# Optimization experiments

Hardware: AMD Instinct MI355X
Metric: run time of the kernel (lower is better)

## Reference

```python
import jax, jax.numpy as jnp
import numpy as np

N = 50000   # nodes
E = 800000  # edges
H = 4       # num_heads
D = 32      # out_dim
IN = 256    # in_dim


def setup_inputs() -> dict:
    key = jax.random.key(0)
    k0, k1, k2, k3, k4, k5 = jax.random.split(key, 6)
    h = jax.random.normal(k0, (N, IN), dtype=jnp.float32)
    # fl weight (torch Linear stores [out, in]), xavier-ish scale
    Wl = jax.random.normal(k1, (H * D, IN), dtype=jnp.float32) * (1.0 / np.sqrt(IN))
    # fc / fq are initialized to small constants in torch; use small random here
    fc = jax.random.normal(k2, (IN, H * D), dtype=jnp.float32) * 0.02
    fq = jax.random.normal(k3, (IN, H * D), dtype=jnp.float32) * 0.02
    src = jax.random.randint(k4, (E,), 0, N)
    dst = jax.random.randint(k5, (E,), 0, N)
    return {"h": h, "Wl": Wl, "fc": fc, "fq": fq, "src": src, "dst": dst}


def reference(h, Wl, fc, fq, src, dst):
    n = h.shape[0]
    ft = (h @ Wl.T).reshape(n, H, D)      # [N,H,D]
    ft_c = (h @ fc).reshape(n, H, D)      # [N,H,D]
    ft_q = (h @ fq).reshape(n, H, D)      # [N,H,D]

    # edge attention: c = ft_c[dst], q = ft_q[src] - c, a = ELU(sum(q*c))
    c = ft_c[dst]                         # [E,H,D]
    a = jax.nn.elu(jnp.sum((ft_q[src] - c) * c, axis=-1))  # [E,H]

    # segmented (per-destination) softmax over incoming edges, per head
    m = jax.ops.segment_max(a, dst, num_segments=n)        # [N,H]
    ex = jnp.exp(a - m[dst])
    s = jax.ops.segment_sum(ex, dst, num_segments=n)       # [N,H]
    attn = ex / s[dst]                                     # [E,H]

    # global top-k (smallest l_s) threshold + mass redistribution, per head
    l_s = int(0.713 * attn.shape[0])
    srt = jnp.sort(attn, axis=0)                           # ascending per head
    thd = srt[l_s - 1]                                     # [H] l_s-th smallest
    topk_sum = jnp.sum(srt[:l_s], axis=0)                  # [H]
    a2 = jnp.where(attn - thd < 0, jnp.zeros((), attn.dtype), attn)
    ratio = (jnp.sum(a2, axis=0) + topk_sum) / jnp.sum(a2, axis=0)  # [H]
    a3 = a2 * ratio                                        # [E,H]

    # weighted scatter-sum of source features to destinations
    out = jax.ops.segment_sum(ft[src] * a3[:, :, None], dst, num_segments=n)  # [N,H,D]

    # concat=True: cat(flattened heads, mean over heads of ft)
    return jnp.concatenate([out.reshape(n, -1), ft.mean(axis=1)], axis=1)  # [N, H*D + D]
```

## Files before the change

### kernel.cpp

```cpp
#include <hip/hip_runtime.h>
#include <hip/hip_bf16.h>
#include <math.h>

#define N_NODES 50000
#define N_EDGES 800000
#define NH 4
#define DH 32
#define IN_DIM 256
#define OUTC 160
#define LS 570400
#define RANK0 (LS - 1)

typedef unsigned long long u64;
#define SC_FX 1099511627776.0

__device__ __forceinline__ unsigned enc_f(float a){
  unsigned u = __float_as_uint(a);
  return (u & 0x80000000u) ? ~u : (u | 0x80000000u);
}
__device__ __forceinline__ float dec_f(unsigned k){
  return (k & 0x80000000u) ? __uint_as_float(k ^ 0x80000000u) : __uint_as_float(~k);
}

__global__ void k_prepw1(const float* __restrict__ Wl, float* __restrict__ W1){
  int i = blockIdx.x * 256 + threadIdx.x;
  if (i >= IN_DIM * 128) return;
  int k = i >> 7, j = i & 127;
  W1[i] = Wl[j * IN_DIM + k];
}
__global__ void k_prepw2(const float* __restrict__ fc, const float* __restrict__ fq,
                         double* __restrict__ W2){
  int i = blockIdx.x * 256 + threadIdx.x;
  if (i >= IN_DIM * 256) return;
  int k = i >> 8, j = i & 255;
  W2[i] = (double)((j < 128) ? fc[k * 128 + j] : fq[k * 128 + (j - 128)]);
}

#define BM 128
#define BK 16
__global__ __launch_bounds__(256) void k_gemm32(const float* __restrict__ A,
                                                const float* __restrict__ W1,
                                                float* __restrict__ C){
  __shared__ float As[BK][BM + 4];
  __shared__ float Bs[BK][128 + 4];
  int tid = threadIdx.x;
  int m0 = blockIdx.x * BM;
  int ty = tid / 16, tx = tid % 16;
  float acc[8][8];
  #pragma unroll
  for (int i = 0; i < 8; i++)
    #pragma unroll
    for (int j = 0; j < 8; j++) acc[i][j] = 0.f;

  for (int k0 = 0; k0 < IN_DIM; k0 += BK){
    #pragma unroll
    for (int i = 0; i < 2; i++){
      int s = tid * 2 + i;
      int row = s >> 2, c4 = s & 3;
      int r = m0 + row;
      float4 v = make_float4(0.f, 0.f, 0.f, 0.f);
      if (r < N_NODES) v = *(const float4*)&A[(size_t)r * IN_DIM + k0 + c4 * 4];
      As[c4 * 4 + 0][row] = v.x; As[c4 * 4 + 1][row] = v.y;
      As[c4 * 4 + 2][row] = v.z; As[c4 * 4 + 3][row] = v.w;
    }
    #pragma unroll
    for (int i = 0; i < 2; i++){
      int s = tid * 2 + i;
      int kr = s >> 5, c4 = s & 31;
      if (c4 < 32){
        float4 v = *(const float4*)&W1[(size_t)(k0 + kr) * 128 + c4 * 4];
        *(float4*)&Bs[kr][c4 * 4] = v;
      }
    }
    __syncthreads();
    #pragma unroll
    for (int kk = 0; kk < BK; kk++){
      float4 a0 = *(const float4*)&As[kk][ty * 4];
      float4 a1 = *(const float4*)&As[kk][64 + ty * 4];
      float4 b0 = *(const float4*)&Bs[kk][tx * 4];
      float4 b1 = *(const float4*)&Bs[kk][64 + tx * 4];
      float av[8] = {a0.x, a0.y, a0.z, a0.w, a1.x, a1.y, a1.z, a1.w};
      float bv[8] = {b0.x, b0.y, b0.z, b0.w, b1.x, b1.y, b1.z, b1.w};
      #pragma unroll
      for (int i = 0; i < 8; i++)
        #pragma unroll
        for (int j = 0; j < 8; j++)
          acc[i][j] = fmaf(av[i], bv[j], acc[i][j]);
    }
    __syncthreads();
  }
  #pragma unroll
  for (int i = 0; i < 8; i++){
    int r = m0 + ((i < 4) ? (ty * 4 + i) : (64 + ty * 4 + (i - 4)));
    if (r >= N_NODES) continue;
    *(float4*)&C[(size_t)r * 128 + tx * 4]      = make_float4(acc[i][0], acc[i][1], acc[i][2], acc[i][3]);
    *(float4*)&C[(size_t)r * 128 + 64 + tx * 4] = make_float4(acc[i][4], acc[i][5], acc[i][6], acc[i][7]);
  }
}

__global__ __launch_bounds__(256) void k_gemm64(const float* __restrict__ A,
                                                const double* __restrict__ W2,
                                                double* __restrict__ C){
  __shared__ double As[16][66];
  __shared__ double Bs[16][66];
  int tid = threadIdx.x;
  int m0 = blockIdx.x * 64;
  int n0 = blockIdx.y * 64;
  int ty = tid / 16, tx = tid % 16;
  double acc[4][4];
  #pragma unroll
  for (int i = 0; i < 4; i++)
    #pragma unroll
    for (int j = 0; j < 4; j++) acc[i][j] = 0.0;

  for (int k0 = 0; k0 < IN_DIM; k0 += 16){
    {
      int row = tid >> 2, c4 = tid & 3;
      int r = m0 + row;
      float4 v = make_float4(0.f, 0.f, 0.f, 0.f);
      if (r < N_NODES) v = *(const float4*)&A[(size_t)r * IN_DIM + k0 + c4 * 4];
      As[c4 * 4 + 0][row] = (double)v.x; As[c4 * 4 + 1][row] = (double)v.y;
      As[c4 * 4 + 2][row] = (double)v.z; As[c4 * 4 + 3][row] = (double)v.w;
    }
    {
      int kr = tid >> 4, c4 = tid & 15;
      const double* p = &W2[(size_t)(k0 + kr) * 256 + n0 + c4 * 4];
      double2 b0 = *(const double2*)p;
      double2 b1 = *(const double2*)(p + 2);
      Bs[kr][c4 * 4 + 0] = b0.x; Bs[kr][c4 * 4 + 1] = b0.y;
      Bs[kr][c4 * 4 + 2] = b1.x; Bs[kr][c4 * 4 + 3] = b1.y;
    }
    __syncthreads();
    #pragma unroll
    for (int kk = 0; kk < 16; kk++){
      double a[4], b[4];
      #pragma unroll
      for (int i = 0; i < 4; i++) a[i] = As[kk][ty * 4 + i];
      #pragma unroll
      for (int j = 0; j < 4; j++) b[j] = Bs[kk][tx * 4 + j];
      #pragma unroll
      for (int i = 0; i < 4; i++)
        #pragma unroll
        for (int j = 0; j < 4; j++)
          acc[i][j] = fma(a[i], b[j], acc[i][j]);
    }
    __syncthreads();
  }
  #pragma unroll
  for (int i = 0; i < 4; i++){
    int r = m0 + ty * 4 + i;
    if (r >= N_NODES) continue;
    double* p = &C[(size_t)r * 256 + n0 + tx * 4];
    *(double2*)p       = make_double2(acc[i][0], acc[i][1]);
    *(double2*)(p + 2) = make_double2(acc[i][2], acc[i][3]);
  }
}

__global__ void k_mean(const float* __restrict__ ft, float* __restrict__ out){
  int i = blockIdx.x * 256 + threadIdx.x;
  if (i >= N_NODES * DH) return;
  int n = i / DH, dd = i % DH;
  const float* p = ft + (size_t)n * 128;
  out[(size_t)n * OUTC + 128 + dd] = 0.25f * (p[dd] + p[32 + dd] + p[64 + dd] + p[96 + dd]);
}

__global__ __launch_bounds__(256) void k_edge_a(const double* __restrict__ fcq,
    const int* __restrict__ src, const int* __restrict__ dst,
    double* __restrict__ abuf, unsigned* __restrict__ menc){
  int wid = blockIdx.x * 4 + (threadIdx.x >> 6);
  int t = threadIdx.x & 63;
  if (wid >= N_EDGES) return;
  int s = src[wid], d = dst[wid];
  const double* qp = fcq + (size_t)s * 256 + 128;
  const double* cp = fcq + (size_t)d * 256;
  double2 q = *(const double2*)&qp[t * 2];
  double2 c = *(const double2*)&cp[t * 2];
  double val = (q.x - c.x) * c.x + (q.y - c.y) * c.y;
  val += __shfl_xor(val, 1);
  val += __shfl_xor(val, 2);
  val += __shfl_xor(val, 4);
  val += __shfl_xor(val, 8);
  if ((t & 15) == 0){
    int hh = t >> 4;
    double a = (val > 0.0) ? val : expm1(val);
    abuf[(size_t)wid * 4 + hh] = a;
    atomicMax(&menc[(size_t)d * 4 + hh], enc_f((float)a));
  }
}

__global__ void k_ex_sum(const int* __restrict__ dst, double* __restrict__ abuf,
                         const unsigned* __restrict__ menc, u64* __restrict__ ssum64){
  int i = blockIdx.x * 256 + threadIdx.x;
  if (i >= N_EDGES * 4) return;
  int e = i >> 2, hh = i & 3;
  int d = dst[e];
  double m = (double)dec_f(menc[(size_t)d * 4 + hh]);
  double ex = exp(abuf[i] - m);
  abuf[i] = ex;
  atomicAdd(&ssum64[(size_t)d * 4 + hh], (u64)llrint(ex * SC_FX));
}

__global__ void k_attn(const int* __restrict__ dst, double* __restrict__ abuf,
                       const u64* __restrict__ ssum64){
  int i = blockIdx.x * 256 + threadIdx.x;
  if (i >= N_EDGES * 4) return;
  int e = i >> 2, hh = i & 3;
  double s = (double)ssum64[(size_t)dst[e] * 4 + hh] * (1.0 / SC_FX);
  abuf[i] = abuf[i] / s;
}

__global__ void k_deg(const int* __restrict__ dst, unsigned* __restrict__ deg){
  int e = blockIdx.x * 256 + threadIdx.x;
  if (e < N_EDGES) atomicAdd(&deg[dst[e]], 1u);
}

__global__ __launch_bounds__(1024) void k_scan(const unsigned* __restrict__ deg,
                                               unsigned* __restrict__ offsets){
  __shared__ unsigned ps[1024];
  int t = threadIdx.x;
  const int CH = (N_NODES + 1023) / 1024;
  int base = t * CH;
  unsigned s = 0;
  for (int i = 0; i < CH; i++){
    int n = base + i;
    if (n < N_NODES) s += deg[n];
  }
  ps[t] = s;
  __syncthreads();
  for (int off = 1; off < 1024; off <<= 1){
    unsigned v = (t >= off) ? ps[t - off] : 0;
    __syncthreads();
    ps[t] += v;
    __syncthreads();
  }
  unsigned ex = (t == 0) ? 0 : ps[t - 1];
  for (int i = 0; i < CH; i++){
    int n = base + i;
    if (n < N_NODES){ offsets[n] = ex; ex += deg[n]; }
  }
  if (t == 1023) offsets[N_NODES] = ps[1023];
}

__global__ void k_cpcur(const unsigned* __restrict__ offsets, unsigned* __restrict__ cur){
  int i = blockIdx.x * 256 + threadIdx.x;
  if (i < N_NODES) cur[i] = offsets[i];
}

__global__ void k_fill(const int* __restrict__ dst, unsigned* __restrict__ cur,
                       unsigned* __restrict__ eidx){
  int e = blockIdx.x * 256 + threadIdx.x;
  if (e < N_EDGES) eidx[atomicAdd(&cur[dst[e]], 1u)] = (unsigned)e;
}

__global__ void k_hist(const double* __restrict__ attn, const u64* __restrict__ sel4,
                       unsigned* __restrict__ hist, u64 maskHi, int shift){
  __shared__ unsigned lh[1024];
  for (int j = threadIdx.x; j < 1024; j += 256) lh[j] = 0;
  __syncthreads();
  int i0 = blockIdx.x * 256 + threadIdx.x;
  int hh = i0 & 3;
  u64 sel = sel4[hh];
  const int total = N_EDGES * 4;
  for (int i = i0; i < total; i += gridDim.x * 256){
    u64 u = (u64)__double_as_longlong(attn[i]);
    if ((u & maskHi) == sel)
      atomicAdd(&lh[hh * 256 + (unsigned)((u >> shift) & 255u)], 1u);
  }
  __syncthreads();
  for (int j = threadIdx.x; j < 1024; j += 256)
    if (lh[j]) atomicAdd(&hist[j], lh[j]);
}

__global__ void k_pick(unsigned* __restrict__ hist, u64* __restrict__ sel4,
                       unsigned* __restrict__ krem, unsigned* __restrict__ cnt, int shift){
  __shared__ unsigned lh[1024];
  int t = threadIdx.x;
  for (int j = t; j < 1024; j += 256){ lh[j] = hist[j]; hist[j] = 0; }
  __syncthreads();
  if (t < 4){
    unsigned kr = krem[t];
    unsigned cum = 0, b = 0;
    for (; b < 256; b++){
      unsigned c = lh[t * 256 + b];
      if (kr < cum + c) break;
      cum += c;
    }
    sel4[t] |= ((u64)b) << shift;
    krem[t]  = kr - cum;
    cnt[t]  += cum;
  }
}

__global__ void k_init(unsigned* __restrict__ krem){
  if (threadIdx.x < 4) krem[threadIdx.x] = RANK0;
}

__global__ __launch_bounds__(256) void k_sums(const double* __restrict__ attn,
                                              const u64* __restrict__ sel4,
                                              u64* __restrict__ gsums){
  int t = threadIdx.x;
  int i0 = blockIdx.x * 256 + t;
  int hh = t & 3;
  double thd = __longlong_as_double((long long)sel4[hh]);
  double al = 0.0, ag = 0.0;
  const int total = N_EDGES * 4;
  for (int i = i0; i < total; i += gridDim.x * 256){
    double v = attn[i];
    if (v < thd) al += v; else ag += v;
  }
  long long ql = llrint(al * SC_FX);
  long long qg = llrint(ag * SC_FX);
  #pragma unroll
  for (int m = 4; m < 64; m <<= 1){
    ql += __shfl_xor(ql, m);
    qg += __shfl_xor(qg, m);
  }
  __shared__ long long sl[16], sg[16];
  int wv = t >> 6;
  if ((t & 63) < 4){ sl[wv * 4 + hh] = ql; sg[wv * 4 + hh] = qg; }
  __syncthreads();
  if (t < 4){
    long long a = sl[t] + sl[4 + t] + sl[8 + t] + sl[12 + t];
    long long b = sg[t] + sg[4 + t] + sg[8 + t] + sg[12 + t];
    if (a) atomicAdd(&gsums[t],     (u64)a);
    if (b) atomicAdd(&gsums[4 + t], (u64)b);
  }
}

__global__ void k_ratio(const u64* __restrict__ sel4, const unsigned* __restrict__ cnt,
                        const u64* __restrict__ gsums, double* __restrict__ trd){
  int t = threadIdx.x;
  if (t < 4){
    double thd = __longlong_as_double((long long)sel4[t]);
    double sless = (double)gsums[t]     * (1.0 / SC_FX);
    double sge   = (double)gsums[4 + t] * (1.0 / SC_FX);
    double topk  = sless + (double)(LS - (int)cnt[t]) * thd;
    trd[t] = thd;
    trd[4 + t] = (sge + topk) / sge;
  }
}

__global__ __launch_bounds__(256) void k_scatter2(const float* __restrict__ ft,
    const int* __restrict__ src, const unsigned* __restrict__ offsets,
    const unsigned* __restrict__ eidx, const double* __restrict__ attn,
    const double* __restrict__ trd, float* __restrict__ out){
  int d = blockIdx.x * 4 + (threadIdx.x >> 6);
  int t = threadIdx.x & 63;
  if (d >= N_NODES) return;
  int hh = t >> 4;
  double thd = trd[hh], ratio = trd[4 + hh];
  unsigned k0 = offsets[d], k1 = offsets[d + 1];
  long long acc0 = 0, acc1 = 0;
  for (unsigned k = k0; k < k1; k++){
    unsigned e = eidx[k];
    double w = attn[(size_t)e * 4 + hh];
    double a3 = (w < thd) ? 0.0 : w * ratio;
    if (__ballot(a3 != 0.0) == 0ull) continue;
    if (a3 != 0.0){
      int s = src[e];
      float2 f = *(const float2*)&ft[(size_t)s * 128 + t * 2];
      acc0 += llrint(a3 * (double)f.x * SC_FX);
      acc1 += llrint(a3 * (double)f.y * SC_FX);
    }
  }
  float* p = &out[(size_t)d * OUTC + t * 2];
  p[0] = (float)((double)acc0 * (1.0 / SC_FX));
  p[1] = (float)((double)acc1 * (1.0 / SC_FX));
}

extern "C" void kernel_launch(void* const* d_in, const int* in_sizes, int n_in,
                              void* d_out, int out_size, void* d_ws, size_t ws_size,
                              hipStream_t stream){
  const float* h  = (const float*)d_in[0];
  const float* Wl = (const float*)d_in[1];
  const float* fc = (const float*)d_in[2];
  const float* fq = (const float*)d_in[3];
  const int* src  = (const int*)d_in[4];
  const int* dst  = (const int*)d_in[5];
  float* out = (float*)d_out;

  char* ws = (char*)d_ws;
  float*  W1    = (float*)(ws);
  double* W2    = (double*)(ws + 131072);
  float*  ft32  = (float*)(ws + 655360);
  double* fcq64 = (double*)(ws + 26255360);
  unsigned* offsets = (unsigned*)(ws + 26255360);
  unsigned* cur     = (unsigned*)(ws + 26455368);
  unsigned* eidx    = (unsigned*)(ws + 26655368);
  double* abuf  = (double*)(ws + 128655360);
  unsigned* menc = (unsigned*)(ws + 154255360);
  u64*    ssum64 = (u64*)(ws + 155055360);
  unsigned* hist = (unsigned*)(ws + 156655360);
  u64*    sel4  = (u64*)(ws + 156659456);
  unsigned* krem = (unsigned*)(ws + 156659488);
  unsigned* cnt  = (unsigned*)(ws + 156659504);
  u64*    gsums = (u64*)(ws + 156659520);
  double* trd   = (double*)(ws + 156659584);

  hipMemsetAsync(menc, 0, 800000, stream);
  hipMemsetAsync(ssum64, 0, 1600000, stream);
  hipMemsetAsync(hist, 0, 4224, stream);
  k_init<<<1, 64, 0, stream>>>(krem);

  k_prepw1<<<(IN_DIM * 128 + 255) / 256, 256, 0, stream>>>(Wl, W1);
  k_prepw2<<<(IN_DIM * 256 + 255) / 256, 256, 0, stream>>>(fc, fq, W2);
  k_gemm32<<<(N_NODES + BM - 1) / BM, 256, 0, stream>>>(h, W1, ft32);
  dim3 g64((N_NODES + 63) / 64, 4);
  k_gemm64<<<g64, 256, 0, stream>>>(h, W2, fcq64);
  k_mean<<<(N_NODES * DH + 255) / 256, 256, 0, stream>>>(ft32, out);

  k_edge_a<<<N_EDGES / 4, 256, 0, stream>>>(fcq64, src, dst, abuf, menc);

  hipMemsetAsync(cur, 0, 200000, stream);
  k_deg<<<(N_EDGES + 255) / 256, 256, 0, stream>>>(dst, cur);
  k_scan<<<1, 1024, 0, stream>>>(cur, offsets);
  k_cpcur<<<(N_NODES + 255) / 256, 256, 0, stream>>>(offsets, cur);
  k_fill<<<(N_EDGES + 255) / 256, 256, 0, stream>>>(dst, cur, eidx);

  k_ex_sum<<<(N_EDGES * 4 + 255) / 256, 256, 0, stream>>>(dst, abuf, menc, ssum64);
  k_attn<<<(N_EDGES * 4 + 255) / 256, 256, 0, stream>>>(dst, abuf, ssum64);

  for (int p = 0; p < 8; p++){
    u64 maskHi = (p == 0) ? 0ull : (~0ull) << (64 - 8 * p);
    int shift = 56 - 8 * p;
    k_hist<<<2048, 256, 0, stream>>>(abuf, sel4, hist, maskHi, shift);
    k_pick<<<1, 256, 0, stream>>>(hist, sel4, krem, cnt, shift);
  }
  k_sums<<<2048, 256, 0, stream>>>(abuf, sel4, gsums);
  k_ratio<<<1, 64, 0, stream>>>(sel4, cnt, gsums, trd);

  k_scatter2<<<(N_NODES + 3) / 4, 256, 0, stream>>>(ft32, src, offsets, eidx, abuf, trd, out);
}
```

Before: 1.108 ms.

## Fuse edge softmax per destination, shorten radix select, drop weight prep kernels

Builds the CSR by destination first, then computes edge scores, per-node max, exp-sum and normalisation in one warp-per-node kernel using LDS, storing attention in CSR order. This replaces the atomic max/sum passes and their buffers. The 8-pass radix select becomes two fused histogram+pick passes (last-block ticket), a candidate compaction, and a per-head finishing kernel. Weight transposes are folded into the GEMM loads, and a float a3 buffer is written for the scatter, which prefetches the next edge. The changes add risks: the LDS cap of 160 edges per node, attention staged in the output buffer, and switching to CSR edge order.

```diff
diff --git a/kernel.cpp b/kernel.cpp
--- a/kernel.cpp
+++ b/kernel.cpp
@@ -10,36 +10,57 @@
 #define OUTC 160
 #define LS 570400
 #define RANK0 (LS - 1)
+#define DEG_CAP 160
 
 typedef unsigned long long u64;
 #define SC_FX 1099511627776.0
 
-__device__ __forceinline__ unsigned enc_f(float a){
-  unsigned u = __float_as_uint(a);
-  return (u & 0x80000000u) ? ~u : (u | 0x80000000u);
-}
-__device__ __forceinline__ float dec_f(unsigned k){
-  return (k & 0x80000000u) ? __uint_as_float(k ^ 0x80000000u) : __uint_as_float(~k);
-}
-
-__global__ void k_prepw1(const float* __restrict__ Wl, float* __restrict__ W1){
-  int i = blockIdx.x * 256 + threadIdx.x;
-  if (i >= IN_DIM * 128) return;
-  int k = i >> 7, j = i & 127;
-  W1[i] = Wl[j * IN_DIM + k];
-}
-__global__ void k_prepw2(const float* __restrict__ fc, const float* __restrict__ fq,
-                         double* __restrict__ W2){
-  int i = blockIdx.x * 256 + threadIdx.x;
-  if (i >= IN_DIM * 256) return;
-  int k = i >> 8, j = i & 255;
-  W2[i] = (double)((j < 128) ? fc[k * 128 + j] : fq[k * 128 + (j - 128)]);
+__global__ void k_deg(const int* __restrict__ dst, unsigned* __restrict__ A){
+  int e = blockIdx.x * 256 + threadIdx.x;
+  if (e < N_EDGES) atomicAdd(&A[dst[e]], 1u);
+}
+
+__global__ __launch_bounds__(1024) void k_scan(unsigned* __restrict__ A){
+  __shared__ unsigned ps[1024];
+  int t = threadIdx.x;
+  const int CH = (N_NODES + 1023) / 1024;
+  int base = t * CH;
+  unsigned s = 0;
+  for (int i = 0; i < CH; i++){ int n = base + i; if (n < N_NODES) s += A[n]; }
+  ps[t] = s;
+  __syncthreads();
+  for (int off = 1; off < 1024; off <<= 1){
+    unsigned v = (t >= off) ? ps[t - off] : 0;
+    __syncthreads();
+    ps[t] += v;
+    __syncthreads();
+  }
+  unsigned ex = (t == 0) ? 0 : ps[t - 1];
+  for (int i = 0; i < CH; i++){
+    int n = base + i;
+    if (n < N_NODES){ unsigned dv = A[n]; A[n] = ex; ex += dv; }
+  }
+}
+
+__global__ void k_fill(const int* __restrict__ dst, unsigned* __restrict__ A,
+                       unsigned* __restrict__ eidx){
+  int e = blockIdx.x * 256 + threadIdx.x;
+  if (e < N_EDGES) eidx[atomicAdd(&A[dst[e]], 1u)] = (unsigned)e;
+}
+
+__global__ void k_init(u64* __restrict__ sel4, unsigned* __restrict__ krem,
+                       unsigned* __restrict__ cnt, unsigned* __restrict__ done,
+                       unsigned* __restrict__ ccnt, u64* __restrict__ gsums){
+  int t = threadIdx.x;
+  if (t < 4){ sel4[t] = 0; krem[t] = RANK0; cnt[t] = 0; ccnt[t] = 0; }
+  if (t < 8) gsums[t] = 0;
+  if (t == 0) done[0] = 0;
 }
 
 #define BM 128
 #define BK 16
 __global__ __launch_bounds__(256) void k_gemm32(const float* __restrict__ A,
-                                                const float* __restrict__ W1,
+                                                const float* __restrict__ Wl,
                                                 float* __restrict__ C){
   __shared__ float As[BK][BM + 4];
   __shared__ float Bs[BK][128 + 4];
@@ -66,11 +87,10 @@
     #pragma unroll
     for (int i = 0; i < 2; i++){
       int s = tid * 2 + i;
-      int kr = s >> 5, c4 = s & 31;
-      if (c4 < 32){
-        float4 v = *(const float4*)&W1[(size_t)(k0 + kr) * 128 + c4 * 4];
-        *(float4*)&Bs[kr][c4 * 4] = v;
-      }
+      int j = s >> 2, c4 = s & 3;
+      float4 v = *(const float4*)&Wl[(size_t)j * IN_DIM + k0 + c4 * 4];
+      Bs[c4 * 4 + 0][j] = v.x; Bs[c4 * 4 + 1][j] = v.y;
+      Bs[c4 * 4 + 2][j] = v.z; Bs[c4 * 4 + 3][j] = v.w;
     }
     __syncthreads();
     #pragma unroll
@@ -99,13 +119,18 @@
 }
 
 __global__ __launch_bounds__(256) void k_gemm64(const float* __restrict__ A,
-                                                const double* __restrict__ W2,
-                                                double* __restrict__ C){
+                                                const float* __restrict__ fc,
+                                                const float* __restrict__ fq,
+                                                double* __restrict__ c64,
+                                                double* __restrict__ q64){
   __shared__ double As[16][66];
   __shared__ double Bs[16][66];
   int tid = threadIdx.x;
   int m0 = blockIdx.x * 64;
   int n0 = blockIdx.y * 64;
+  const float* Bsrc = (n0 < 128) ? fc : fq;
+  int j0 = (n0 < 128) ? n0 : n0 - 128;
+  double* Cp = (n0 < 128) ? c64 : q64;
   int ty = tid / 16, tx = tid % 16;
   double acc[4][4];
   #pragma unroll
@@ -124,11 +149,9 @@
     }
     {
       int kr = tid >> 4, c4 = tid & 15;
-      const double* p = &W2[(size_t)(k0 + kr) * 256 + n0 + c4 * 4];
-      double2 b0 = *(const double2*)p;
-      double2 b1 = *(const double2*)(p + 2);
-      Bs[kr][c4 * 4 + 0] = b0.x; Bs[kr][c4 * 4 + 1] = b0.y;
-      Bs[kr][c4 * 4 + 2] = b1.x; Bs[kr][c4 * 4 + 3] = b1.y;
+      float4 v = *(const float4*)&Bsrc[(size_t)(k0 + kr) * 128 + j0 + c4 * 4];
+      Bs[kr][c4 * 4 + 0] = (double)v.x; Bs[kr][c4 * 4 + 1] = (double)v.y;
+      Bs[kr][c4 * 4 + 2] = (double)v.z; Bs[kr][c4 * 4 + 3] = (double)v.w;
     }
     __syncthreads();
     #pragma unroll
@@ -150,116 +173,67 @@
   for (int i = 0; i < 4; i++){
     int r = m0 + ty * 4 + i;
     if (r >= N_NODES) continue;
-    double* p = &C[(size_t)r * 256 + n0 + tx * 4];
+    double* p = &Cp[(size_t)r * 128 + j0 + tx * 4];
     *(double2*)p       = make_double2(acc[i][0], acc[i][1]);
     *(double2*)(p + 2) = make_double2(acc[i][2], acc[i][3]);
   }
 }
 
-__global__ void k_mean(const float* __restrict__ ft, float* __restrict__ out){
-  int i = blockIdx.x * 256 + threadIdx.x;
-  if (i >= N_NODES * DH) return;
-  int n = i / DH, dd = i % DH;
-  const float* p = ft + (size_t)n * 128;
-  out[(size_t)n * OUTC + 128 + dd] = 0.25f * (p[dd] + p[32 + dd] + p[64 + dd] + p[96 + dd]);
-}
-
-__global__ __launch_bounds__(256) void k_edge_a(const double* __restrict__ fcq,
-    const int* __restrict__ src, const int* __restrict__ dst,
-    double* __restrict__ abuf, unsigned* __restrict__ menc){
-  int wid = blockIdx.x * 4 + (threadIdx.x >> 6);
+__global__ __launch_bounds__(256) void k_softedge(const double* __restrict__ c64,
+    const double* __restrict__ q64, const int* __restrict__ src,
+    const unsigned* __restrict__ A, const unsigned* __restrict__ eidx,
+    double* __restrict__ abuf){
+  __shared__ double lds_a[4][DEG_CAP * 4];
+  int d = blockIdx.x * 4 + (threadIdx.x >> 6);
   int t = threadIdx.x & 63;
-  if (wid >= N_EDGES) return;
-  int s = src[wid], d = dst[wid];
-  const double* qp = fcq + (size_t)s * 256 + 128;
-  const double* cp = fcq + (size_t)d * 256;
-  double2 q = *(const double2*)&qp[t * 2];
-  double2 c = *(const double2*)&cp[t * 2];
-  double val = (q.x - c.x) * c.x + (q.y - c.y) * c.y;
-  val += __shfl_xor(val, 1);
-  val += __shfl_xor(val, 2);
-  val += __shfl_xor(val, 4);
-  val += __shfl_xor(val, 8);
-  if ((t & 15) == 0){
-    int hh = t >> 4;
+  int wv = threadIdx.x >> 6;
+  if (d >= N_NODES) return;
+  unsigned k0 = d ? A[d - 1] : 0u, k1 = A[d];
+  if (k0 == k1) return;
+  double2 c = *(const double2*)&c64[(size_t)d * 128 + t * 2];
+  double m = -1.0e300;
+  int sn = src[eidx[k0]];
+  double2 qn = *(const double2*)&q64[(size_t)sn * 128 + t * 2];
+  for (unsigned k = k0; k < k1; k++){
+    double2 q = qn;
+    if (k + 1 < k1){
+      int s2 = src[eidx[k + 1]];
+      qn = *(const double2*)&q64[(size_t)s2 * 128 + t * 2];
+    }
+    double val = (q.x - c.x) * c.x + (q.y - c.y) * c.y;
+    val += __shfl_xor(val, 1);
+    val += __shfl_xor(val, 2);
+    val += __shfl_xor(val, 4);
+    val += __shfl_xor(val, 8);
     double a = (val > 0.0) ? val : expm1(val);
-    abuf[(size_t)wid * 4 + hh] = a;
-    atomicMax(&menc[(size_t)d * 4 + hh], enc_f((float)a));
-  }
-}
-
-__global__ void k_ex_sum(const int* __restrict__ dst, double* __restrict__ abuf,
-                         const unsigned* __restrict__ menc, u64* __restrict__ ssum64){
-  int i = blockIdx.x * 256 + threadIdx.x;
-  if (i >= N_EDGES * 4) return;
-  int e = i >> 2, hh = i & 3;
-  int d = dst[e];
-  double m = (double)dec_f(menc[(size_t)d * 4 + hh]);
-  double ex = exp(abuf[i] - m);
-  abuf[i] = ex;
-  atomicAdd(&ssum64[(size_t)d * 4 + hh], (u64)llrint(ex * SC_FX));
-}
-
-__global__ void k_attn(const int* __restrict__ dst, double* __restrict__ abuf,
-                       const u64* __restrict__ ssum64){
-  int i = blockIdx.x * 256 + threadIdx.x;
-  if (i >= N_EDGES * 4) return;
-  int e = i >> 2, hh = i & 3;
-  double s = (double)ssum64[(size_t)dst[e] * 4 + hh] * (1.0 / SC_FX);
-  abuf[i] = abuf[i] / s;
-}
-
-__global__ void k_deg(const int* __restrict__ dst, unsigned* __restrict__ deg){
-  int e = blockIdx.x * 256 + threadIdx.x;
-  if (e < N_EDGES) atomicAdd(&deg[dst[e]], 1u);
-}
-
-__global__ __launch_bounds__(1024) void k_scan(const unsigned* __restrict__ deg,
-                                               unsigned* __restrict__ offsets){
-  __shared__ unsigned ps[1024];
-  int t = threadIdx.x;
-  const int CH = (N_NODES + 1023) / 1024;
-  int base = t * CH;
-  unsigned s = 0;
-  for (int i = 0; i < CH; i++){
-    int n = base + i;
-    if (n < N_NODES) s += deg[n];
-  }
-  ps[t] = s;
-  __syncthreads();
-  for (int off = 1; off < 1024; off <<= 1){
-    unsigned v = (t >= off) ? ps[t - off] : 0;
-    __syncthreads();
-    ps[t] += v;
-    __syncthreads();
-  }
-  unsigned ex = (t == 0) ? 0 : ps[t - 1];
-  for (int i = 0; i < CH; i++){
-    int n = base + i;
-    if (n < N_NODES){ offsets[n] = ex; ex += deg[n]; }
-  }
-  if (t == 1023) offsets[N_NODES] = ps[1023];
-}
-
-__global__ void k_cpcur(const unsigned* __restrict__ offsets, unsigned* __restrict__ cur){
-  int i = blockIdx.x * 256 + threadIdx.x;
-  if (i < N_NODES) cur[i] = offsets[i];
-}
-
-__global__ void k_fill(const int* __restrict__ dst, unsigned* __restrict__ cur,
-                       unsigned* __restrict__ eidx){
-  int e = blockIdx.x * 256 + threadIdx.x;
-  if (e < N_EDGES) eidx[atomicAdd(&cur[dst[e]], 1u)] = (unsigned)e;
-}
-
-__global__ void k_hist(const double* __restrict__ attn, const u64* __restrict__ sel4,
-                       unsigned* __restrict__ hist, u64 maskHi, int shift){
+    m = fmax(m, a);
+    if ((t & 15) == 0) lds_a[wv][(k - k0) * 4 + (t >> 4)] = a;
+  }
+  double mm = __shfl(m, (t & 3) * 16);
+  unsigned nj = (k1 - k0) * 4;
+  long long sfx = 0;
+  for (unsigned jj = t; jj < nj; jj += 64){
+    double ex = exp(lds_a[wv][jj] - mm);
+    lds_a[wv][jj] = ex;
+    sfx += llrint(ex * SC_FX);
+  }
+  #pragma unroll
+  for (int msk = 4; msk < 64; msk <<= 1) sfx += __shfl_xor(sfx, msk);
+  double sd = (double)sfx * (1.0 / SC_FX);
+  for (unsigned jj = t; jj < nj; jj += 64)
+    abuf[(size_t)k0 * 4 + jj] = lds_a[wv][jj] / sd;
+}
+
+__global__ __launch_bounds__(256) void k_hp(const double* __restrict__ attn,
+    u64* __restrict__ sel4, unsigned* __restrict__ krem, unsigned* __restrict__ cnt,
+    unsigned* __restrict__ hist, unsigned* __restrict__ done, u64 maskHi, int shift){
   __shared__ unsigned lh[1024];
+  __shared__ unsigned ticket;
   for (int j = threadIdx.x; j < 1024; j += 256) lh[j] = 0;
   __syncthreads();
   int i0 = blockIdx.x * 256 + threadIdx.x;
   int hh = i0 & 3;
-  u64 sel = sel4[hh];
+  u64 sel = sel4[hh] & maskHi;
   const int total = N_EDGES * 4;
   for (int i = i0; i < total; i += gridDim.x * 256){
     u64 u = (u64)__double_as_longlong(attn[i]);
@@ -269,35 +243,86 @@
   __syncthreads();
   for (int j = threadIdx.x; j < 1024; j += 256)
     if (lh[j]) atomicAdd(&hist[j], lh[j]);
-}
-
-__global__ void k_pick(unsigned* __restrict__ hist, u64* __restrict__ sel4,
-                       unsigned* __restrict__ krem, unsigned* __restrict__ cnt, int shift){
-  __shared__ unsigned lh[1024];
+  __threadfence();
+  if (threadIdx.x == 0) ticket = atomicAdd(done, 1u);
+  __syncthreads();
+  if (ticket == gridDim.x - 1){
+    __threadfence();
+    for (int j = threadIdx.x; j < 1024; j += 256){ lh[j] = hist[j]; hist[j] = 0; }
+    __syncthreads();
+    if (threadIdx.x < 4){
+      int t = threadIdx.x;
+      unsigned kr = krem[t], cum = 0, b = 0;
+      for (; b < 256; b++){
+        unsigned c2 = lh[t * 256 + b];
+        if (kr < cum + c2) break;
+        cum += c2;
+      }
+      sel4[t] |= ((u64)b) << shift;
+      krem[t] = kr - cum;
+      cnt[t] += cum;
+    }
+    if (threadIdx.x == 0) *done = 0;
+  }
+}
+
+__global__ void k_compact(const double* __restrict__ attn, const u64* __restrict__ sel4,
+                          unsigned* __restrict__ ccnt, double* __restrict__ cand){
+  int i0 = blockIdx.x * 256 + threadIdx.x;
+  int hh = i0 & 3;
+  u64 sel = sel4[hh] & 0xFFFF000000000000ull;
+  const int total = N_EDGES * 4;
+  for (int i = i0; i < total; i += gridDim.x * 256){
+    double v = attn[i];
+    u64 u = (u64)__double_as_longlong(v);
+    if ((u & 0xFFFF000000000000ull) == sel){
+      unsigned pos = atomicAdd(&ccnt[hh], 1u);
+      cand[(size_t)hh * N_EDGES + pos] = v;
+    }
+  }
+}
+
+__global__ __launch_bounds__(256) void k_finish(const double* __restrict__ cand,
+    const unsigned* __restrict__ ccnt, u64* __restrict__ sel4,
+    unsigned* __restrict__ krem, unsigned* __restrict__ cnt){
+  __shared__ unsigned lh[256];
+  __shared__ u64 s_sel;
+  __shared__ unsigned s_krem, s_cnt;
+  int h = blockIdx.x;
   int t = threadIdx.x;
-  for (int j = t; j < 1024; j += 256){ lh[j] = hist[j]; hist[j] = 0; }
-  __syncthreads();
-  if (t < 4){
-    unsigned kr = krem[t];
-    unsigned cum = 0, b = 0;
-    for (; b < 256; b++){
-      unsigned c = lh[t * 256 + b];
-      if (kr < cum + c) break;
-      cum += c;
-    }
-    sel4[t] |= ((u64)b) << shift;
-    krem[t]  = kr - cum;
-    cnt[t]  += cum;
-  }
-}
-
-__global__ void k_init(unsigned* __restrict__ krem){
-  if (threadIdx.x < 4) krem[threadIdx.x] = RANK0;
+  if (t == 0){ s_sel = sel4[h]; s_krem = krem[h]; s_cnt = cnt[h]; }
+  __syncthreads();
+  unsigned n = ccnt[h];
+  const double* cp = cand + (size_t)h * N_EDGES;
+  for (int p = 2; p < 8; p++){
+    int shift = 56 - 8 * p;
+    u64 maskHi = ~((1ull << (shift + 8)) - 1);
+    lh[t] = 0;
+    __syncthreads();
+    u64 sel = s_sel;
+    for (unsigned i = t; i < n; i += 256){
+      u64 u = (u64)__double_as_longlong(cp[i]);
+      if ((u & maskHi) == sel) atomicAdd(&lh[(unsigned)((u >> shift) & 255u)], 1u);
+    }
+    __syncthreads();
+    if (t == 0){
+      unsigned kr = s_krem, cum = 0, b = 0;
+      for (; b < 256; b++){
+        unsigned c2 = lh[b];
+        if (kr < cum + c2) break;
+        cum += c2;
+      }
+      s_sel |= ((u64)b) << shift;
+      s_krem = kr - cum;
+      s_cnt += cum;
+    }
+    __syncthreads();
+  }
+  if (t == 0){ sel4[h] = s_sel; krem[h] = s_krem; cnt[h] = s_cnt; }
 }
 
 __global__ __launch_bounds__(256) void k_sums(const double* __restrict__ attn,
-                                              const u64* __restrict__ sel4,
-                                              u64* __restrict__ gsums){
+    const u64* __restrict__ sel4, u64* __restrict__ gsums, float* __restrict__ a3){
   int t = threadIdx.x;
   int i0 = blockIdx.x * 256 + t;
   int hh = t & 3;
@@ -306,7 +331,8 @@
   const int total = N_EDGES * 4;
   for (int i = i0; i < total; i += gridDim.x * 256){
     double v = attn[i];
-    if (v < thd) al += v; else ag += v;
+    if (v < thd){ al += v; a3[i] = 0.f; }
+    else        { ag += v; a3[i] = (float)v; }
   }
   long long ql = llrint(al * SC_FX);
   long long qg = llrint(ag * SC_FX);
@@ -341,31 +367,42 @@
 }
 
 __global__ __launch_bounds__(256) void k_scatter2(const float* __restrict__ ft,
-    const int* __restrict__ src, const unsigned* __restrict__ offsets,
-    const unsigned* __restrict__ eidx, const double* __restrict__ attn,
+    const int* __restrict__ src, const unsigned* __restrict__ A,
+    const unsigned* __restrict__ eidx, const float* __restrict__ a3,
     const double* __restrict__ trd, float* __restrict__ out){
   int d = blockIdx.x * 4 + (threadIdx.x >> 6);
   int t = threadIdx.x & 63;
   if (d >= N_NODES) return;
   int hh = t >> 4;
-  double thd = trd[hh], ratio = trd[4 + hh];
-  unsigned k0 = offsets[d], k1 = offsets[d + 1];
+  double ratio = trd[4 + hh];
+  unsigned k0 = d ? A[d - 1] : 0u, k1 = A[d];
   long long acc0 = 0, acc1 = 0;
+  float wn = (k0 < k1) ? a3[(size_t)k0 * 4 + hh] : 0.f;
+  unsigned en = (k0 < k1) ? eidx[k0] : 0u;
   for (unsigned k = k0; k < k1; k++){
-    unsigned e = eidx[k];
-    double w = attn[(size_t)e * 4 + hh];
-    double a3 = (w < thd) ? 0.0 : w * ratio;
-    if (__ballot(a3 != 0.0) == 0ull) continue;
-    if (a3 != 0.0){
+    float w = wn;
+    unsigned e = en;
+    if (k + 1 < k1){ wn = a3[(size_t)(k + 1) * 4 + hh]; en = eidx[k + 1]; }
+    if (__ballot(w != 0.f) == 0ull) continue;
+    if (w != 0.f){
       int s = src[e];
       float2 f = *(const float2*)&ft[(size_t)s * 128 + t * 2];
-      acc0 += llrint(a3 * (double)f.x * SC_FX);
-      acc1 += llrint(a3 * (double)f.y * SC_FX);
+      double a3r = (double)w * ratio;
+      acc0 += llrint(a3r * (double)f.x * SC_FX);
+      acc1 += llrint(a3r * (double)f.y * SC_FX);
     }
   }
   float* p = &out[(size_t)d * OUTC + t * 2];
   p[0] = (float)((double)acc0 * (1.0 / SC_FX));
   p[1] = (float)((double)acc1 * (1.0 / SC_FX));
+}
+
+__global__ void k_mean(const float* __restrict__ ft, float* __restrict__ out){
+  int i = blockIdx.x * 256 + threadIdx.x;
+  if (i >= N_NODES * DH) return;
+  int n = i / DH, dd = i % DH;
+  const float* p = ft + (size_t)n * 128;
+  out[(size_t)n * OUTC + 128 + dd] = 0.25f * (p[dd] + p[32 + dd] + p[64 + dd] + p[96 + dd]);
 }
 
 extern "C" void kernel_launch(void* const* d_in, const int* in_sizes, int n_in,
@@ -380,54 +417,47 @@
   float* out = (float*)d_out;
 
   char* ws = (char*)d_ws;
-  float*  W1    = (float*)(ws);
-  double* W2    = (double*)(ws + 131072);
-  float*  ft32  = (float*)(ws + 655360);
-  double* fcq64 = (double*)(ws + 26255360);
-  unsigned* offsets = (unsigned*)(ws + 26255360);
-  unsigned* cur     = (unsigned*)(ws + 26455368);
-  unsigned* eidx    = (unsigned*)(ws + 26655368);
-  double* abuf  = (double*)(ws + 128655360);
-  unsigned* menc = (unsigned*)(ws + 154255360);
-  u64*    ssum64 = (u64*)(ws + 155055360);
-  unsigned* hist = (unsigned*)(ws + 156655360);
-  u64*    sel4  = (u64*)(ws + 156659456);
-  unsigned* krem = (unsigned*)(ws + 156659488);
-  unsigned* cnt  = (unsigned*)(ws + 156659504);
-  u64*    gsums = (u64*)(ws + 156659520);
-  double* trd   = (double*)(ws + 156659584);
-
-  hipMemsetAsync(menc, 0, 800000, stream);
-  hipMemsetAsync(ssum64, 0, 1600000, stream);
-  hipMemsetAsync(hist, 0, 4224, stream);
-  k_init<<<1, 64, 0, stream>>>(krem);
-
-  k_prepw1<<<(IN_DIM * 128 + 255) / 256, 256, 0, stream>>>(Wl, W1);
-  k_prepw2<<<(IN_DIM * 256 + 255) / 256, 256, 0, stream>>>(fc, fq, W2);
-  k_gemm32<<<(N_NODES + BM - 1) / BM, 256, 0, stream>>>(h, W1, ft32);
+  float*  ft32 = (float*)(ws);
+  double* c64  = (double*)(ws + 25600000);
+  float*  a3   = (float*)(ws + 25600000);
+  double* q64  = (double*)(ws + 76800000);
+  double* cand = (double*)(ws + 76800000);
+  unsigned* A    = (unsigned*)(ws + 128000000);
+  unsigned* eidx = (unsigned*)(ws + 128200064);
+  unsigned* hist = (unsigned*)(ws + 131400064);
+  u64*    sel4  = (u64*)(ws + 131404160);
+  unsigned* krem = (unsigned*)(ws + 131404192);
+  unsigned* cnt  = (unsigned*)(ws + 131404208);
+  unsigned* done = (unsigned*)(ws + 131404224);
+  unsigned* ccnt = (unsigned*)(ws + 131404240);
+  u64*    gsums = (u64*)(ws + 131404256);
+  double* trd   = (double*)(ws + 131404320);
+
+  double* abuf = (double*)d_out;
+
+  hipMemsetAsync(A, 0, 200004, stream);
+  hipMemsetAsync(hist, 0, 4096, stream);
+  k_init<<<1, 64, 0, stream>>>(sel4, krem, cnt, done, ccnt, gsums);
+
+  k_deg<<<(N_EDGES + 255) / 256, 256, 0, stream>>>(dst, A);
+  k_scan<<<1, 1024, 0, stream>>>(A);
+  k_fill<<<(N_EDGES + 255) / 256, 256, 0, stream>>>(dst, A, eidx);
+
+  k_gemm32<<<(N_NODES + BM - 1) / BM, 256, 0, stream>>>(h, Wl, ft32);
   dim3 g64((N_NODES + 63) / 64, 4);
-  k_gemm64<<<g64, 256, 0, stream>>>(h, W2, fcq64);
+  k_gemm64<<<g64, 256, 0, stream>>>(h, fc, fq, c64, q64);
+
+  k_softedge<<<(N_NODES + 3) / 4, 256, 0, stream>>>(c64, q64, src, A, eidx, abuf);
+
+  k_hp<<<1024, 256, 0, stream>>>(abuf, sel4, krem, cnt, hist, done, 0ull, 56);
+  k_hp<<<1024, 256, 0, stream>>>(abuf, sel4, krem, cnt, hist, done,
+                                 0xFF00000000000000ull, 48);
+  k_compact<<<2048, 256, 0, stream>>>(abuf, sel4, ccnt, cand);
+  k_finish<<<4, 256, 0, stream>>>(cand, ccnt, sel4, krem, cnt);
+
+  k_sums<<<2048, 256, 0, stream>>>(abuf, sel4, gsums, a3);
+  k_ratio<<<1, 64, 0, stream>>>(sel4, cnt, gsums, trd);
+
+  k_scatter2<<<(N_NODES + 3) / 4, 256, 0, stream>>>(ft32, src, A, eidx, a3, trd, out);
   k_mean<<<(N_NODES * DH + 255) / 256, 256, 0, stream>>>(ft32, out);
-
-  k_edge_a<<<N_EDGES / 4, 256, 0, stream>>>(fcq64, src, dst, abuf, menc);
-
-  hipMemsetAsync(cur, 0, 200000, stream);
-  k_deg<<<(N_EDGES + 255) / 256, 256, 0, stream>>>(dst, cur);
-  k_scan<<<1, 1024, 0, stream>>>(cur, offsets);
-  k_cpcur<<<(N_NODES + 255) / 256, 256, 0, stream>>>(offsets, cur);
-  k_fill<<<(N_EDGES + 255) / 256, 256, 0, stream>>>(dst, cur, eidx);
-
-  k_ex_sum<<<(N_EDGES * 4 + 255) / 256, 256, 0, stream>>>(dst, abuf, menc, ssum64);
-  k_attn<<<(N_EDGES * 4 + 255) / 256, 256, 0, stream>>>(dst, abuf, ssum64);
-
-  for (int p = 0; p < 8; p++){
-    u64 maskHi = (p == 0) ? 0ull : (~0ull) << (64 - 8 * p);
-    int shift = 56 - 8 * p;
-    k_hist<<<2048, 256, 0, stream>>>(abuf, sel4, hist, maskHi, shift);
-    k_pick<<<1, 256, 0, stream>>>(hist, sel4, krem, cnt, shift);
-  }
-  k_sums<<<2048, 256, 0, stream>>>(abuf, sel4, gsums);
-  k_ratio<<<1, 64, 0, stream>>>(sel4, cnt, gsums, trd);
-
-  k_scatter2<<<(N_NODES + 3) / 4, 256, 0, stream>>>(ft32, src, offsets, eidx, abuf, trd, out);
-}
+}
```

Measured after the change: 2.296 ms. 107% more time.
